# Kernel optimization log

Measured on AMD Instinct MI355X. Metric: run time of the kernel, lower is better.

## Reference

```python
import jax, jax.numpy as jnp
import numpy as np

N = 20000      # num_nodes
E = 256000     # num_edges (before self loops)
D_IN = 128
HID = 128      # hidden_dim (per-head out channels)
HEADS = 4
T = 2          # num_timesteps
NEG_SLOPE = 0.2
LN_EPS = 1e-5


def setup_inputs() -> dict:
    key = jax.random.key(0)
    ks = jax.random.split(key, 24)
    def rn(k, shape, s=0.05):
        return jax.random.normal(k, shape, jnp.float32) * s
    HH = HEADS * HID  # 512
    return {
        "x": jax.random.normal(ks[0], (N, D_IN), jnp.float32),
        "edge_index": jax.random.randint(ks[1], (2, E), 0, N),
        # input projection
        "Wp": rn(ks[2], (HID, D_IN)), "bp": jnp.zeros((HID,), jnp.float32),
        # GAT layer 0: in=HID, heads=HEADS, concat
        "W0": rn(ks[3], (HH, HID)), "as0": rn(ks[4], (HEADS, HID)), "ad0": rn(ks[5], (HEADS, HID)), "b0": jnp.zeros((HH,), jnp.float32),
        # GAT layer 1: in=HH, heads=HEADS, concat
        "W1": rn(ks[6], (HH, HH)), "as1": rn(ks[7], (HEADS, HID)), "ad1": rn(ks[8], (HEADS, HID)), "b1": jnp.zeros((HH,), jnp.float32),
        # GAT layer 2 (last): in=HH, heads=1, concat=False
        "W2": rn(ks[9], (HID, HH)), "as2": rn(ks[10], (1, HID)), "ad2": rn(ks[11], (1, HID)), "b2": jnp.zeros((HID,), jnp.float32),
        # layer norms (dims 512, 512, 128)
        "g0": jnp.ones((HH,), jnp.float32), "be0": jnp.zeros((HH,), jnp.float32),
        "g1": jnp.ones((HH,), jnp.float32), "be1": jnp.zeros((HH,), jnp.float32),
        "g2": jnp.ones((HID,), jnp.float32), "be2": jnp.zeros((HID,), jnp.float32),
        # temporal MultiheadAttention (embed=HID, 4 heads)
        "Wqkv": rn(ks[12], (3 * HID, HID)), "bqkv": jnp.zeros((3 * HID,), jnp.float32),
        "Wo": rn(ks[13], (HID, HID)), "bo": jnp.zeros((HID,), jnp.float32),
    }


def _layernorm(x, g, b):
    mu = x.mean(-1, keepdims=True)
    var = ((x - mu) ** 2).mean(-1, keepdims=True)
    return (x - mu) * jax.lax.rsqrt(var + LN_EPS) * g + b


def _gat_conv(h, src, dst, W, a_src, a_dst, bias, heads, concat):
    # h: [N, in]; W: [heads*HID, in]; a_src/a_dst: [heads, HID]
    xp = (h @ W.T).reshape(N, heads, HID)            # [N, heads, HID]
    al_s = (xp * a_src).sum(-1)                      # [N, heads]
    al_d = (xp * a_dst).sum(-1)                      # [N, heads]
    e = jax.nn.leaky_relu(al_s[src] + al_d[dst], NEG_SLOPE)  # [Etot, heads]
    m = jax.ops.segment_max(e, dst, num_segments=N)          # segment softmax over dst
    e = jnp.exp(e - m[dst])
    s = jax.ops.segment_sum(e, dst, num_segments=N)
    alpha = e / (s[dst] + 1e-16)                     # [Etot, heads]
    msg = xp[src] * alpha[:, :, None]                # [Etot, heads, HID]
    out = jax.ops.segment_sum(msg, dst, num_segments=N)      # [N, heads, HID]
    out = out.reshape(N, heads * HID) if concat else out.mean(1)
    return out + bias


def _forward(x, edge_index, Wp, bp, W0, as0, ad0, b0, W1, as1, ad1, b1,
             W2, as2, ad2, b2, g0, be0, g1, be1, g2, be2, Wqkv, bqkv, Wo, bo):
    loops = jnp.arange(N, dtype=edge_index.dtype)    # add_self_loops=True
    src = jnp.concatenate([edge_index[0], loops])
    dst = jnp.concatenate([edge_index[1], loops])

    h = x @ Wp.T + bp                                 # [N, HID]
    layers = [
        (W0, as0, ad0, b0, HEADS, True, g0, be0),
        (W1, as1, ad1, b1, HEADS, True, g1, be1),
        (W2, as2, ad2, b2, 1, False, g2, be2),
    ]
    states = []
    for t in range(T):
        h_t = h
        for i, (W, a_s, a_d, b, heads, concat, g, be) in enumerate(layers):
            h_res = h_t
            h_t = _gat_conv(h_t, src, dst, W, a_s, a_d, b, heads, concat)
            h_t = jax.nn.elu(h_t)
            h_t = _layernorm(h_t, g, be)
            # dropout is identity in eval mode
            if i > 0:
                if h_res.shape[-1] != h_t.shape[-1]:
                    # adaptive_avg_pool1d 512 -> 128: mean over groups of 4
                    r = h_res.shape[-1] // h_t.shape[-1]
                    h_res = h_res.reshape(N, h_t.shape[-1], r).mean(-1)
                h_t = h_t + h_res
        states.append(h_t)
        h = h_t

    ts = jnp.stack(states, axis=1)                    # [N, T, HID]
    # temporal self-attention (4 heads, head_dim = HID//4)
    nh, hd = 4, HID // 4
    qkv = ts @ Wqkv.T + bqkv                          # [N, T, 3*HID]
    q, k, v = jnp.split(qkv, 3, axis=-1)
    q = q.reshape(N, T, nh, hd).transpose(0, 2, 1, 3)
    k = k.reshape(N, T, nh, hd).transpose(0, 2, 1, 3)
    v = v.reshape(N, T, nh, hd).transpose(0, 2, 1, 3)
    attn = jax.nn.softmax(jnp.einsum("nhqd,nhkd->nhqk", q, k) / jnp.sqrt(jnp.float32(hd)), axis=-1)
    o = jnp.einsum("nhqk,nhkd->nhqd", attn, v).transpose(0, 2, 1, 3).reshape(N, T, HID)
    o = o @ Wo.T + bo
    return o.mean(axis=1)                             # [N, HID]


def reference(x, edge_index, Wp, bp, W0, as0, ad0, b0, W1, as1, ad1, b1,
              W2, as2, ad2, b2, g0, be0, g1, be1, g2, be2, Wqkv, bqkv, Wo, bo):
    return _forward(x, edge_index, Wp, bp, W0, as0, ad0, b0, W1, as1, ad1, b1,
                    W2, as2, ad2, b2, g0, be0, g1, be1, g2, be2, Wqkv, bqkv, Wo, bo)
```

## Files before the change

kernel.cpp:

```cpp
#include <hip/hip_runtime.h>
#include <math.h>

#define N_NODES 20000
#define N_EDGES 256000
#define ETOT (N_EDGES + N_NODES)
#define NPAD 20096
#define NPAD2 40064
#define NBLK_SCAN ((N_NODES + 255) / 256)

typedef __attribute__((ext_vector_type(8))) short bf16x8;
typedef __attribute__((ext_vector_type(4))) float f32x4;

__device__ __forceinline__ unsigned short f2bf(float f) {
    unsigned int u = __builtin_bit_cast(unsigned int, f);
    u = (u + 0x7fff + ((u >> 16) & 1)) >> 16;
    return (unsigned short)u;
}

__device__ __forceinline__ float bf2f(unsigned short u) {
    return __builtin_bit_cast(float, (unsigned int)u << 16);
}

__device__ __forceinline__ void gload_lds16(const void* g, void* l) {
    __builtin_amdgcn_global_load_lds(
        (const __attribute__((address_space(1))) void*)g,
        (__attribute__((address_space(3))) void*)l, 16, 0, 0);
}

__device__ __forceinline__ void fma8(float* acc, uint4 v, float w) {
    acc[0] = fmaf(w, __builtin_bit_cast(float, v.x << 16), acc[0]);
    acc[1] = fmaf(w, __builtin_bit_cast(float, v.x & 0xffff0000u), acc[1]);
    acc[2] = fmaf(w, __builtin_bit_cast(float, v.y << 16), acc[2]);
    acc[3] = fmaf(w, __builtin_bit_cast(float, v.y & 0xffff0000u), acc[3]);
    acc[4] = fmaf(w, __builtin_bit_cast(float, v.z << 16), acc[4]);
    acc[5] = fmaf(w, __builtin_bit_cast(float, v.z & 0xffff0000u), acc[5]);
    acc[6] = fmaf(w, __builtin_bit_cast(float, v.w << 16), acc[6]);
    acc[7] = fmaf(w, __builtin_bit_cast(float, v.w & 0xffff0000u), acc[7]);
}


__global__ void hist_kernel(const int* __restrict__ ei, int* __restrict__ cnt) {
    for (int e = blockIdx.x * blockDim.x + threadIdx.x; e < ETOT;
         e += gridDim.x * blockDim.x) {
        int d = (e < N_EDGES) ? ei[N_EDGES + e] : (e - N_EDGES);
        atomicAdd(&cnt[d], 1);
    }
}

__global__ __launch_bounds__(256) void scanA(const int* __restrict__ cnt,
                                             int* __restrict__ incl,
                                             int* __restrict__ bsum) {
    __shared__ int sh[256];
    int t = threadIdx.x;
    int i = blockIdx.x * 256 + t;
    int v = (i < N_NODES) ? cnt[i] : 0;
    sh[t] = v;
    __syncthreads();
#pragma unroll
    for (int off = 1; off < 256; off <<= 1) {
        int u = (t >= off) ? sh[t - off] : 0;
        __syncthreads();
        sh[t] += u;
        __syncthreads();
    }
    if (i < N_NODES) incl[i] = sh[t];
    if (t == 255) bsum[blockIdx.x] = sh[255];
}

__global__ __launch_bounds__(128) void scanB(int* __restrict__ bsum,
                                             int* __restrict__ row_start) {
    __shared__ int sh[128];
    int t = threadIdx.x;
    int v = (t < NBLK_SCAN) ? bsum[t] : 0;
    sh[t] = v;
    __syncthreads();
#pragma unroll
    for (int off = 1; off < 128; off <<= 1) {
        int u = (t >= off) ? sh[t - off] : 0;
        __syncthreads();
        sh[t] += u;
        __syncthreads();
    }
    if (t < NBLK_SCAN) bsum[t] = sh[t] - v;
    if (t == 0) row_start[0] = 0;
}

__global__ __launch_bounds__(256) void scanC(int* __restrict__ cursor,
                                             int* __restrict__ row_start,
                                             const int* __restrict__ bsum) {
    int i = blockIdx.x * 256 + threadIdx.x;
    if (i < N_NODES) {
        int incl = row_start[i + 1] + bsum[blockIdx.x];
        row_start[i + 1] = incl;
        cursor[i] = incl - cursor[i];
    }
}

__global__ void scatter_kernel(const int* __restrict__ ei, int* __restrict__ cursor,
                               int* __restrict__ sorted_id) {
    for (int e = blockIdx.x * blockDim.x + threadIdx.x; e < ETOT;
         e += gridDim.x * blockDim.x) {
        int d = (e < N_EDGES) ? ei[N_EDGES + e] : (e - N_EDGES);
        int pos = atomicAdd(&cursor[d], 1);
        sorted_id[pos] = e;
    }
}

__global__ __launch_bounds__(256) void segsort_kernel(
    const int* __restrict__ ei, const int* __restrict__ row_start,
    int* __restrict__ sorted_id, int* __restrict__ sorted_src) {
    int wv = threadIdx.x >> 6, lane = threadIdx.x & 63;
    int n = blockIdx.x * 4 + wv;
    if (n >= N_NODES) return;
    int base = row_start[n];
    int deg = row_start[n + 1] - base;
    if (deg <= 64) {
        int id = (lane < deg) ? sorted_id[base + lane] : 0x7fffffff;
        int rank = 0;
        for (int j = 0; j < deg; j++) {
            int idj = __shfl(id, j);
            rank += (idj < id);
        }
        if (lane < deg) {
            int src = (id < N_EDGES) ? ei[id] : (id - N_EDGES);
            sorted_src[base + rank] = src;
        }
    } else if (lane == 0) {
        for (int i = base + 1; i < base + deg; i++) {
            int v = sorted_id[i];
            int j = i - 1;
            while (j >= base && sorted_id[j] > v) {
                sorted_id[j + 1] = sorted_id[j];
                j--;
            }
            sorted_id[j + 1] = v;
        }
        for (int i = base; i < base + deg; i++) {
            int id = sorted_id[i];
            sorted_src[i] = (id < N_EDGES) ? ei[id] : (id - N_EDGES);
        }
    }
}

struct SetupArgs {
    const float* s[7];
    unsigned short* d[7];
    int cum[8];
    int* cursor;
    unsigned short* x16;
    unsigned short* h16n;
    unsigned short* h16wA;
    unsigned short* h16wB;
    unsigned short* xp16;
    unsigned short* st16;
    unsigned short* om16;
};

__global__ __launch_bounds__(256) void setup_all(SetupArgs a) {
    int i = blockIdx.x * 256 + threadIdx.x;
    const int PR = NPAD - N_NODES;
    if (i < N_NODES) a.cursor[i] = 0;
    if (i < PR * 128) {
        a.x16[(size_t)N_NODES * 128 + i] = 0;
        a.h16n[(size_t)N_NODES * 128 + i] = 0;
        a.om16[(size_t)N_NODES * 128 + i] = 0;
    }
    if (i < PR * 512) {
        a.h16wA[(size_t)N_NODES * 512 + i] = 0;
        a.h16wB[(size_t)N_NODES * 512 + i] = 0;
        a.xp16[(size_t)N_NODES * 512 + i] = 0;
    }
    if (i < (NPAD2 - 2 * N_NODES) * 128) a.st16[(size_t)(2 * N_NODES) * 128 + i] = 0;
    if (i < a.cum[7]) {
        int r = 0;
        while (i >= a.cum[r + 1]) r++;
        int off = i - a.cum[r];
        a.d[r][off] = f2bf(a.s[r][off]);
    }
}

__global__ __launch_bounds__(512) void make_ahat(
    const unsigned short* __restrict__ W016, const float* __restrict__ as0,
    const float* __restrict__ ad0, float* __restrict__ ahat_s,
    float* __restrict__ ahat_d) {
    int t = threadIdx.x;
    int h = t >> 7, k = t & 127;
    float ss = 0.f, sd = 0.f;
    for (int c = 0; c < 128; c++) {
        float w = bf2f(W016[(size_t)(h * 128 + c) * 128 + k]);
        ss = fmaf(as0[h * 128 + c], w, ss);
        sd = fmaf(ad0[h * 128 + c], w, sd);
    }
    ahat_s[t] = ss;
    ahat_d[t] = sd;
}

__global__ __launch_bounds__(256) void coef128(
    const unsigned short* __restrict__ h16n, const float* __restrict__ ahat_s,
    const float* __restrict__ ahat_d, float* __restrict__ als,
    float* __restrict__ ald) {
    int wv = threadIdx.x >> 6, lane = threadIdx.x & 63;
    int n = blockIdx.x * 4 + wv;
    if (n >= N_NODES) return;
    int k0 = 2 * lane;
    float h0 = bf2f(h16n[(size_t)n * 128 + k0]);
    float h1 = bf2f(h16n[(size_t)n * 128 + k0 + 1]);
    float accs[4], accd[4];
#pragma unroll
    for (int h = 0; h < 4; h++) {
        accs[h] = h0 * ahat_s[h * 128 + k0] + h1 * ahat_s[h * 128 + k0 + 1];
        accd[h] = h0 * ahat_d[h * 128 + k0] + h1 * ahat_d[h * 128 + k0 + 1];
    }
#pragma unroll
    for (int off = 1; off <= 32; off <<= 1) {
#pragma unroll
        for (int h = 0; h < 4; h++) {
            accs[h] += __shfl_xor(accs[h], off);
            accd[h] += __shfl_xor(accd[h], off);
        }
    }
    if (lane == 0) {
#pragma unroll
        for (int h = 0; h < 4; h++) {
            als[n * 4 + h] = accs[h];
            ald[n * 4 + h] = accd[h];
        }
    }
}

__global__ __launch_bounds__(256) void gemm_mfma(
    const unsigned short* __restrict__ A, const unsigned short* __restrict__ B,
    const float* __restrict__ bias, float* __restrict__ Cf,
    unsigned short* __restrict__ C16, int R, int K, int ldc,
    const float* __restrict__ a_s, const float* __restrict__ a_d,
    float* __restrict__ al_s, float* __restrict__ al_d, int H,
    int lda, int adiag) {
    __shared__ unsigned short Al[64 * 64];
    __shared__ unsigned short Bl[128 * 64];
    __shared__ float red_s[4][32], red_d[4][32];
    int tid = threadIdx.x;
    int lane = tid & 63, wv = tid >> 6;
    int wr = (wv >> 1) * 32, wc = (wv & 1) * 64;
    size_t br = (size_t)blockIdx.x * 64;
    size_t bc = (size_t)blockIdx.y * 128;
    int acol = adiag ? (int)blockIdx.y * K : 0;
    f32x4 acc[2][4] = {};
    for (int k0 = 0; k0 < K; k0 += 64) {
#pragma unroll
        for (int i = 0; i < 2; i++) {
            int idx = i * 256 + tid;
            int row = idx >> 3;
            int kb = (idx & 7) << 4;
            gload_lds16((const char*)(A + (br + row) * lda + acol + k0) + kb,
                        (char*)Al + idx * 16);
        }
#pragma unroll
        for (int i = 0; i < 4; i++) {
            int idx = i * 256 + tid;
            int row = idx >> 3;
            int kb = (idx & 7) << 4;
            gload_lds16((const char*)(B + (bc + row) * K + k0) + kb,
                        (char*)Bl + idx * 16);
        }
        __syncthreads();
#pragma unroll
        for (int kk = 0; kk < 2; kk++) {
            bf16x8 af[2], bfr[4];
#pragma unroll
            for (int m = 0; m < 2; m++)
                af[m] = *(const bf16x8*)&Al[(wr + m * 16 + (lane & 15)) * 64 +
                                            kk * 32 + (lane >> 4) * 8];
#pragma unroll
            for (int n = 0; n < 4; n++)
                bfr[n] = *(const bf16x8*)&Bl[(wc + n * 16 + (lane & 15)) * 64 +
                                             kk * 32 + (lane >> 4) * 8];
#pragma unroll
            for (int m = 0; m < 2; m++)
#pragma unroll
                for (int n = 0; n < 4; n++)
                    acc[m][n] = __builtin_amdgcn_mfma_f32_16x16x32_bf16(
                        af[m], bfr[n], acc[m][n], 0, 0, 0);
        }
        __syncthreads();
    }

    if (al_s) {
        float asr[4], adr[4];
#pragma unroll
        for (int n = 0; n < 4; n++) {
            int c = (int)bc + wc + n * 16 + (lane & 15);
            asr[n] = a_s[c];
            adr[n] = a_d[c];
        }
        float ps[2][4], pd[2][4];
#pragma unroll
        for (int m = 0; m < 2; m++)
#pragma unroll
            for (int j = 0; j < 4; j++) {
                float s = 0.f, d = 0.f;
#pragma unroll
                for (int n = 0; n < 4; n++) {
                    float v = acc[m][n][j];
                    s = fmaf(v, asr[n], s);
                    d = fmaf(v, adr[n], d);
                }
#pragma unroll
                for (int off = 8; off; off >>= 1) {
                    s += __shfl_xor(s, off);
                    d += __shfl_xor(d, off);
                }
                ps[m][j] = s;
                pd[m][j] = d;
            }
        if ((lane & 15) == 0) {
#pragma unroll
            for (int m = 0; m < 2; m++)
#pragma unroll
                for (int j = 0; j < 4; j++) {
                    int lr = m * 16 + (lane >> 4) * 4 + j;
                    red_s[wv][lr] = ps[m][j];
                    red_d[wv][lr] = pd[m][j];
                }
        }
        __syncthreads();
        if (tid < 64) {
            int half = tid >> 5, lr = tid & 31;
            float s = red_s[half * 2][lr] + red_s[half * 2 + 1][lr];
            float d = red_d[half * 2][lr] + red_d[half * 2 + 1][lr];
            size_t r = br + half * 32 + lr;
            if (r < (size_t)R) {
                al_s[r * H + blockIdx.y] = s;
                al_d[r * H + blockIdx.y] = d;
            }
        }
    }

#pragma unroll
    for (int m = 0; m < 2; m++) {
        int r0 = wr + m * 16 + (lane >> 4) * 4;
#pragma unroll
        for (int n = 0; n < 4; n++) {
            int c = (int)bc + wc + n * 16 + (lane & 15);
            float bv = bias ? bias[c] : 0.f;
#pragma unroll
            for (int j = 0; j < 4; j++) {
                size_t r = br + r0 + j;
                if (r < (size_t)R) {
                    float v = acc[m][n][j] + bv;
                    if (Cf) Cf[r * ldc + c] = v;
                    if (C16) C16[r * ldc + c] = f2bf(v);
                }
            }
        }
    }
}

template <int RES>
__global__ __launch_bounds__(256) void gat_agg512(
    const unsigned short* __restrict__ xp16, const float* __restrict__ al_s,
    const float* __restrict__ al_d, const int* __restrict__ row_start,
    const int* __restrict__ srcs, const float* __restrict__ bias,
    const float* __restrict__ gamma, const float* __restrict__ beta,
    const unsigned short* __restrict__ h_res16, unsigned short* __restrict__ out16) {
    const int C = 512;
    int tid = threadIdx.x;
    int lane = tid & 63, wv = tid >> 6;
    int n = blockIdx.x * 4 + wv;
    __shared__ int offw[4][64];
    __shared__ float logw[4][256];
    if (n >= N_NODES) return;
    int base = row_start[n];
    int deg = row_start[n + 1] - base;
    int head = lane >> 4;

    float acc[8] = {};
    float scale_end;

    if (deg <= 64) {
        int e_ = lane >> 2, h_ = lane & 3;
        float m = -3.4e38f;
        for (int e0 = 0; e0 < deg; e0 += 16) {
            int e = e0 + e_;
            float v = -3.4e38f;
            if (e < deg) {
                int src = srcs[base + e];
                if (h_ == 0) offw[wv][e] = src * (C * 2);
                float t = al_s[src * 4 + h_] + al_d[n * 4 + h_];
                v = t > 0.f ? t : 0.2f * t;
                logw[wv][e * 4 + h_] = v;
            }
            m = fmaxf(m, v);
        }
#pragma unroll
        for (int off = 4; off <= 32; off <<= 1) m = fmaxf(m, __shfl_xor(m, off));
        float s = 0.f;
        for (int e0 = 0; e0 < deg; e0 += 16) {
            int e = e0 + e_;
            if (e < deg) {
                float p = __expf(logw[wv][e * 4 + h_] - m);
                logw[wv][e * 4 + h_] = p;
                s += p;
            }
        }
#pragma unroll
        for (int off = 4; off <= 32; off <<= 1) s += __shfl_xor(s, off);
        float inv = 1.0f / (s + 1e-16f);
        scale_end = __shfl(inv, head);
        const char* xb = (const char*)xp16 + lane * 16;
#pragma unroll 4
        for (int j = 0; j < deg; j++) {
            float w = logw[wv][j * 4 + head];
            uint4 vv = *(const uint4*)(xb + offw[wv][j]);
            fma8(acc, vv, w);
        }
    } else {
        int e_ = lane >> 2, h_ = lane & 3;
        float m = -3.4e38f;
        for (int e0 = 0; e0 < deg; e0 += 16) {
            int e = e0 + e_;
            if (e < deg) {
                int src = srcs[base + e];
                float t = al_s[src * 4 + h_] + al_d[n * 4 + h_];
                t = t > 0.f ? t : 0.2f * t;
                m = fmaxf(m, t);
            }
        }
#pragma unroll
        for (int off = 4; off <= 32; off <<= 1) m = fmaxf(m, __shfl_xor(m, off));
        float s = 0.f;
        for (int e0 = 0; e0 < deg; e0 += 16) {
            int e = e0 + e_;
            if (e < deg) {
                int src = srcs[base + e];
                float t = al_s[src * 4 + h_] + al_d[n * 4 + h_];
                t = t > 0.f ? t : 0.2f * t;
                s += __expf(t - m);
            }
        }
#pragma unroll
        for (int off = 4; off <= 32; off <<= 1) s += __shfl_xor(s, off);
        float mg = __shfl(m, head);
        float sg = __shfl(s, head);
        float invg = 1.0f / (sg + 1e-16f);
        float aldh = al_d[n * 4 + head];
        const char* xb = (const char*)xp16 + lane * 16;
        for (int j = 0; j < deg; j++) {
            int src = srcs[base + j];
            float t = al_s[src * 4 + head] + aldh;
            t = t > 0.f ? t : 0.2f * t;
            float w = __expf(t - mg) * invg;
            uint4 vv = *(const uint4*)(xb + (size_t)src * (C * 2));
            fma8(acc, vv, w);
        }
        scale_end = 1.0f;
    }

    int ch0 = 8 * lane;
    float vals[8];
    {
        float4 b0 = *(const float4*)&bias[ch0];
        float4 b1 = *(const float4*)&bias[ch0 + 4];
        vals[0] = acc[0] * scale_end + b0.x;
        vals[1] = acc[1] * scale_end + b0.y;
        vals[2] = acc[2] * scale_end + b0.z;
        vals[3] = acc[3] * scale_end + b0.w;
        vals[4] = acc[4] * scale_end + b1.x;
        vals[5] = acc[5] * scale_end + b1.y;
        vals[6] = acc[6] * scale_end + b1.z;
        vals[7] = acc[7] * scale_end + b1.w;
    }
    float s2 = 0.f, q = 0.f;
#pragma unroll
    for (int k = 0; k < 8; k++) {
        vals[k] = vals[k] > 0.f ? vals[k] : (__expf(vals[k]) - 1.0f);
        s2 += vals[k];
        q += vals[k] * vals[k];
    }
#pragma unroll
    for (int off = 1; off <= 32; off <<= 1) {
        s2 += __shfl_xor(s2, off);
        q += __shfl_xor(q, off);
    }
    float mu = s2 / C;
    float var = q / C - mu * mu;
    float rstd = 1.0f / sqrtf(var + 1e-5f);
    {
        float4 g0 = *(const float4*)&gamma[ch0];
        float4 g1 = *(const float4*)&gamma[ch0 + 4];
        float4 be0v = *(const float4*)&beta[ch0];
        float4 be1v = *(const float4*)&beta[ch0 + 4];
        float gg[8] = {g0.x, g0.y, g0.z, g0.w, g1.x, g1.y, g1.z, g1.w};
        float bb[8] = {be0v.x, be0v.y, be0v.z, be0v.w,
                       be1v.x, be1v.y, be1v.z, be1v.w};
#pragma unroll
        for (int k = 0; k < 8; k++) vals[k] = (vals[k] - mu) * rstd * gg[k] + bb[k];
    }
    if (RES == 1) {
        ushort4 r0 = *(const ushort4*)&h_res16[(size_t)n * C + ch0];
        ushort4 r1 = *(const ushort4*)&h_res16[(size_t)n * C + ch0 + 4];
        vals[0] += bf2f(r0.x); vals[1] += bf2f(r0.y);
        vals[2] += bf2f(r0.z); vals[3] += bf2f(r0.w);
        vals[4] += bf2f(r1.x); vals[5] += bf2f(r1.y);
        vals[6] += bf2f(r1.z); vals[7] += bf2f(r1.w);
    }
    uint4 pk;
    pk.x = (unsigned)f2bf(vals[0]) | ((unsigned)f2bf(vals[1]) << 16);
    pk.y = (unsigned)f2bf(vals[2]) | ((unsigned)f2bf(vals[3]) << 16);
    pk.z = (unsigned)f2bf(vals[4]) | ((unsigned)f2bf(vals[5]) << 16);
    pk.w = (unsigned)f2bf(vals[6]) | ((unsigned)f2bf(vals[7]) << 16);
    *(uint4*)&out16[(size_t)n * C + ch0] = pk;
}

__global__ __launch_bounds__(256) void gat_gather128(
    const unsigned short* __restrict__ h16n, const float* __restrict__ al_s,
    const float* __restrict__ al_d, const int* __restrict__ row_start,
    const int* __restrict__ srcs, unsigned short* __restrict__ s16) {
    int tid = threadIdx.x;
    int lane = tid & 63, wv = tid >> 6;
    int n = blockIdx.x * 4 + wv;
    __shared__ int offw[4][64];
    __shared__ float logw[4][256];
    if (n >= N_NODES) return;
    int base = row_start[n];
    int deg = row_start[n + 1] - base;
    int head = lane >> 4;
    int li = lane & 15;

    float acc[8] = {};
    float scale_end;

    if (deg <= 64) {
        int e_ = lane >> 2, h_ = lane & 3;
        float m = -3.4e38f;
        for (int e0 = 0; e0 < deg; e0 += 16) {
            int e = e0 + e_;
            float v = -3.4e38f;
            if (e < deg) {
                int src = srcs[base + e];
                if (h_ == 0) offw[wv][e] = src * 256;
                float t = al_s[src * 4 + h_] + al_d[n * 4 + h_];
                v = t > 0.f ? t : 0.2f * t;
                logw[wv][e * 4 + h_] = v;
            }
            m = fmaxf(m, v);
        }
#pragma unroll
        for (int off = 4; off <= 32; off <<= 1) m = fmaxf(m, __shfl_xor(m, off));
        float s = 0.f;
        for (int e0 = 0; e0 < deg; e0 += 16) {
            int e = e0 + e_;
            if (e < deg) {
                float p = __expf(logw[wv][e * 4 + h_] - m);
                logw[wv][e * 4 + h_] = p;
                s += p;
            }
        }
#pragma unroll
        for (int off = 4; off <= 32; off <<= 1) s += __shfl_xor(s, off);
        float inv = 1.0f / (s + 1e-16f);
        scale_end = __shfl(inv, head);
        const char* xb = (const char*)h16n + li * 16;
#pragma unroll 4
        for (int j = 0; j < deg; j++) {
            float w = logw[wv][j * 4 + head];
            uint4 vv = *(const uint4*)(xb + offw[wv][j]);
            fma8(acc, vv, w);
        }
    } else {
        int e_ = lane >> 2, h_ = lane & 3;
        float m = -3.4e38f;
        for (int e0 = 0; e0 < deg; e0 += 16) {
            int e = e0 + e_;
            if (e < deg) {
                int src = srcs[base + e];
                float t = al_s[src * 4 + h_] + al_d[n * 4 + h_];
                t = t > 0.f ? t : 0.2f * t;
                m = fmaxf(m, t);
            }
        }
#pragma unroll
        for (int off = 4; off <= 32; off <<= 1) m = fmaxf(m, __shfl_xor(m, off));
        float s = 0.f;
        for (int e0 = 0; e0 < deg; e0 += 16) {
            int e = e0 + e_;
            if (e < deg) {
                int src = srcs[base + e];
                float t = al_s[src * 4 + h_] + al_d[n * 4 + h_];
                t = t > 0.f ? t : 0.2f * t;
                s += __expf(t - m);
            }
        }
#pragma unroll
        for (int off = 4; off <= 32; off <<= 1) s += __shfl_xor(s, off);
        float mg = __shfl(m, head);
        float sg = __shfl(s, head);
        float invg = 1.0f / (sg + 1e-16f);
        float aldh = al_d[n * 4 + head];
        const char* xb = (const char*)h16n + li * 16;
        for (int j = 0; j < deg; j++) {
            int src = srcs[base + j];
            float t = al_s[src * 4 + head] + aldh;
            t = t > 0.f ? t : 0.2f * t;
            float w = __expf(t - mg) * invg;
            uint4 vv = *(const uint4*)(xb + (size_t)src * 256);
            fma8(acc, vv, w);
        }
        scale_end = 1.0f;
    }

    uint4 pk;
    pk.x = (unsigned)f2bf(acc[0] * scale_end) | ((unsigned)f2bf(acc[1] * scale_end) << 16);
    pk.y = (unsigned)f2bf(acc[2] * scale_end) | ((unsigned)f2bf(acc[3] * scale_end) << 16);
    pk.z = (unsigned)f2bf(acc[4] * scale_end) | ((unsigned)f2bf(acc[5] * scale_end) << 16);
    pk.w = (unsigned)f2bf(acc[6] * scale_end) | ((unsigned)f2bf(acc[7] * scale_end) << 16);
    *(uint4*)&s16[(size_t)n * 512 + 8 * lane] = pk;
}

__global__ __launch_bounds__(256) void ln512(
    const unsigned short* __restrict__ proj16, const float* __restrict__ bias,
    const float* __restrict__ gamma, const float* __restrict__ beta,
    unsigned short* __restrict__ out16) {
    const int C = 512;
    int lane = threadIdx.x & 63, wv = threadIdx.x >> 6;
    int n = blockIdx.x * 4 + wv;
    if (n >= N_NODES) return;
    int ch0 = 8 * lane;
    uint4 pv = *(const uint4*)&proj16[(size_t)n * C + ch0];
    float4 b0 = *(const float4*)&bias[ch0];
    float4 b1 = *(const float4*)&bias[ch0 + 4];
    float vals[8];
    vals[0] = __builtin_bit_cast(float, pv.x << 16) + b0.x;
    vals[1] = __builtin_bit_cast(float, pv.x & 0xffff0000u) + b0.y;
    vals[2] = __builtin_bit_cast(float, pv.y << 16) + b0.z;
    vals[3] = __builtin_bit_cast(float, pv.y & 0xffff0000u) + b0.w;
    vals[4] = __builtin_bit_cast(float, pv.z << 16) + b1.x;
    vals[5] = __builtin_bit_cast(float, pv.z & 0xffff0000u) + b1.y;
    vals[6] = __builtin_bit_cast(float, pv.w << 16) + b1.z;
    vals[7] = __builtin_bit_cast(float, pv.w & 0xffff0000u) + b1.w;
    float s2 = 0.f, q = 0.f;
#pragma unroll
    for (int k = 0; k < 8; k++) {
        vals[k] = vals[k] > 0.f ? vals[k] : (__expf(vals[k]) - 1.0f);
        s2 += vals[k];
        q += vals[k] * vals[k];
    }
#pragma unroll
    for (int off = 1; off <= 32; off <<= 1) {
        s2 += __shfl_xor(s2, off);
        q += __shfl_xor(q, off);
    }
    float mu = s2 / C;
    float var = q / C - mu * mu;
    float rstd = 1.0f / sqrtf(var + 1e-5f);
    float4 g0 = *(const float4*)&gamma[ch0];
    float4 g1 = *(const float4*)&gamma[ch0 + 4];
    float4 be0v = *(const float4*)&beta[ch0];
    float4 be1v = *(const float4*)&beta[ch0 + 4];
    float gg[8] = {g0.x, g0.y, g0.z, g0.w, g1.x, g1.y, g1.z, g1.w};
    float bb[8] = {be0v.x, be0v.y, be0v.z, be0v.w, be1v.x, be1v.y, be1v.z, be1v.w};
#pragma unroll
    for (int k = 0; k < 8; k++) vals[k] = (vals[k] - mu) * rstd * gg[k] + bb[k];
    uint4 pk;
    pk.x = (unsigned)f2bf(vals[0]) | ((unsigned)f2bf(vals[1]) << 16);
    pk.y = (unsigned)f2bf(vals[2]) | ((unsigned)f2bf(vals[3]) << 16);
    pk.z = (unsigned)f2bf(vals[4]) | ((unsigned)f2bf(vals[5]) << 16);
    pk.w = (unsigned)f2bf(vals[6]) | ((unsigned)f2bf(vals[7]) << 16);
    *(uint4*)&out16[(size_t)n * C + ch0] = pk;
}

__global__ __launch_bounds__(64) void gat_agg128(
    const unsigned short* __restrict__ xp16, const float* __restrict__ al_s,
    const float* __restrict__ al_d, const int* __restrict__ row_start,
    const int* __restrict__ srcs, const float* __restrict__ bias,
    const float* __restrict__ gamma, const float* __restrict__ beta,
    const unsigned short* __restrict__ h_res16, unsigned short* __restrict__ out16,
    unsigned short* __restrict__ out2_16, int out2_stride) {
    const int C = 128;
    int n = blockIdx.x;
    int lane = threadIdx.x & 63;
    __shared__ int off_sh[64];
    __shared__ float w_sh[64];
    __shared__ float m_sh, s_sh;
    int base = row_start[n];
    int deg = row_start[n + 1] - base;

    float acc[8] = {};

    if (deg <= 64) {
        float v = -3.4e38f;
        if (lane < deg) {
            int src = srcs[base + lane];
            off_sh[lane] = src * (C * 2);
            float t = al_s[src] + al_d[n];
            v = t > 0.f ? t : 0.2f * t;
        }
        float m = v;
#pragma unroll
        for (int off = 32; off; off >>= 1) m = fmaxf(m, __shfl_xor(m, off));
        float p = (lane < deg) ? __expf(v - m) : 0.f;
        float s = p;
#pragma unroll
        for (int off = 32; off; off >>= 1) s += __shfl_xor(s, off);
        s += 1e-16f;
        if (lane < deg) w_sh[lane] = p / s;
        __syncthreads();
        int li = lane & 15, rg = lane >> 4;
        const char* xb = (const char*)xp16 + li * 16;
        for (int j = rg; j < deg; j += 4) {
            uint4 vv = *(const uint4*)(xb + off_sh[j]);
            fma8(acc, vv, w_sh[j]);
        }
    } else {
        float ald = al_d[n];
        float m = -3.4e38f;
        for (int e = lane; e < deg; e += 64) {
            float v = al_s[srcs[base + e]] + ald;
            v = v > 0.f ? v : 0.2f * v;
            m = fmaxf(m, v);
        }
#pragma unroll
        for (int off = 32; off; off >>= 1) m = fmaxf(m, __shfl_xor(m, off));
        float s = 0.f;
        for (int e = lane; e < deg; e += 64) {
            float v = al_s[srcs[base + e]] + ald;
            v = v > 0.f ? v : 0.2f * v;
            s += __expf(v - m);
        }
#pragma unroll
        for (int off = 32; off; off >>= 1) s += __shfl_xor(s, off);
        if (lane == 0) { m_sh = m; s_sh = s + 1e-16f; }
        __syncthreads();
        float mh = m_sh, ssh = s_sh;
        int li = lane & 15, rg = lane >> 4;
        const char* xb = (const char*)xp16 + li * 16;
        for (int j = rg; j < deg; j += 4) {
            int src = srcs[base + j];
            float t = al_s[src] + ald;
            t = t > 0.f ? t : 0.2f * t;
            float w = __expf(t - mh) / ssh;
            uint4 vv = *(const uint4*)(xb + (size_t)src * (C * 2));
            fma8(acc, vv, w);
        }
    }

#pragma unroll
    for (int k = 0; k < 8; k++) {
        acc[k] += __shfl_xor(acc[k], 16);
        acc[k] += __shfl_xor(acc[k], 32);
    }
    int li = lane & 15;
    int ch0 = 8 * li;
    float vals[8];
    float4 b0 = *(const float4*)&bias[ch0];
    float4 b1 = *(const float4*)&bias[ch0 + 4];
    vals[0] = acc[0] + b0.x; vals[1] = acc[1] + b0.y;
    vals[2] = acc[2] + b0.z; vals[3] = acc[3] + b0.w;
    vals[4] = acc[4] + b1.x; vals[5] = acc[5] + b1.y;
    vals[6] = acc[6] + b1.z; vals[7] = acc[7] + b1.w;
    float s = 0.f, q = 0.f;
#pragma unroll
    for (int k = 0; k < 8; k++) {
        vals[k] = vals[k] > 0.f ? vals[k] : (__expf(vals[k]) - 1.0f);
        s += vals[k];
        q += vals[k] * vals[k];
    }
#pragma unroll
    for (int off = 8; off; off >>= 1) {
        s += __shfl_xor(s, off);
        q += __shfl_xor(q, off);
    }
    float mu = s / C;
    float var = q / C - mu * mu;
    float rstd = 1.0f / sqrtf(var + 1e-5f);
    float4 g0 = *(const float4*)&gamma[ch0];
    float4 g1 = *(const float4*)&gamma[ch0 + 4];
    float4 be0v = *(const float4*)&beta[ch0];
    float4 be1v = *(const float4*)&beta[ch0 + 4];
    float gg[8] = {g0.x, g0.y, g0.z, g0.w, g1.x, g1.y, g1.z, g1.w};
    float bb[8] = {be0v.x, be0v.y, be0v.z, be0v.w, be1v.x, be1v.y, be1v.z, be1v.w};
#pragma unroll
    for (int k = 0; k < 8; k++) vals[k] = (vals[k] - mu) * rstd * gg[k] + bb[k];
    {
        const unsigned short* r = &h_res16[(size_t)n * 512 + 4 * ch0];
#pragma unroll
        for (int k = 0; k < 8; k++) {
            ushort4 rv = *(const ushort4*)&r[4 * k];
            vals[k] += 0.25f * (bf2f(rv.x) + bf2f(rv.y) + bf2f(rv.z) + bf2f(rv.w));
        }
    }
    if (lane < 16) {
        uint4 pk;
        pk.x = (unsigned)f2bf(vals[0]) | ((unsigned)f2bf(vals[1]) << 16);
        pk.y = (unsigned)f2bf(vals[2]) | ((unsigned)f2bf(vals[3]) << 16);
        pk.z = (unsigned)f2bf(vals[4]) | ((unsigned)f2bf(vals[5]) << 16);
        pk.w = (unsigned)f2bf(vals[6]) | ((unsigned)f2bf(vals[7]) << 16);
        if (out16) *(uint4*)&out16[(size_t)n * C + ch0] = pk;
        if (out2_16) *(uint4*)&out2_16[(size_t)n * out2_stride + ch0] = pk;
    }
}

__global__ __launch_bounds__(128) void temporal_attn(
    const unsigned short* __restrict__ qkv16, unsigned short* __restrict__ om16) {
    __shared__ float sh[768];
    int n = blockIdx.x;
    int c = threadIdx.x;
    for (int i = c; i < 768; i += 128) {
        int t = i / 384;
        sh[i] = bf2f(qkv16[(size_t)(n * 2 + t) * 384 + (i - t * 384)]);
    }
    __syncthreads();
    int head = c >> 5;
    int hb = head * 32;
    const float scale = 0.17677669529663687f;
    float o[2];
#pragma unroll
    for (int qt = 0; qt < 2; qt++) {
        float s0 = 0.f, s1 = 0.f;
#pragma unroll
        for (int d = 0; d < 32; d++) {
            float qv = sh[qt * 384 + hb + d];
            s0 = fmaf(qv, sh[0 * 384 + 128 + hb + d], s0);
            s1 = fmaf(qv, sh[1 * 384 + 128 + hb + d], s1);
        }
        s0 *= scale; s1 *= scale;
        float m = fmaxf(s0, s1);
        float p0 = __expf(s0 - m), p1 = __expf(s1 - m);
        float inv = 1.0f / (p0 + p1);
        o[qt] = p0 * inv * sh[0 * 384 + 256 + c] + p1 * inv * sh[1 * 384 + 256 + c];
    }
    om16[(size_t)n * 128 + c] = f2bf(0.5f * (o[0] + o[1]));
}


extern "C" void kernel_launch(void* const* d_in, const int* in_sizes, int n_in,
                              void* d_out, int out_size, void* d_ws, size_t ws_size,
                              hipStream_t stream) {
    const float* x   = (const float*)d_in[0];
    const int*   ei  = (const int*)d_in[1];
    const float* Wp  = (const float*)d_in[2];
    const float* bp  = (const float*)d_in[3];
    const float* W0  = (const float*)d_in[4];
    const float* as0 = (const float*)d_in[5];
    const float* ad0 = (const float*)d_in[6];
    const float* b0  = (const float*)d_in[7];
    const float* W1  = (const float*)d_in[8];
    const float* as1 = (const float*)d_in[9];
    const float* ad1 = (const float*)d_in[10];
    const float* b1  = (const float*)d_in[11];
    const float* W2  = (const float*)d_in[12];
    const float* as2 = (const float*)d_in[13];
    const float* ad2 = (const float*)d_in[14];
    const float* b2  = (const float*)d_in[15];
    const float* g0  = (const float*)d_in[16];
    const float* be0 = (const float*)d_in[17];
    const float* g1  = (const float*)d_in[18];
    const float* be1 = (const float*)d_in[19];
    const float* g2  = (const float*)d_in[20];
    const float* be2 = (const float*)d_in[21];
    const float* Wqkv = (const float*)d_in[22];
    const float* bqkv = (const float*)d_in[23];
    const float* Wo  = (const float*)d_in[24];
    const float* bo  = (const float*)d_in[25];
    float* out = (float*)d_out;

    const int N = N_NODES;
    float* f = (float*)d_ws;
    float* als = f;
    float* ald = als + (size_t)N * 4;
    float* ahat_s = ald + (size_t)N * 4;
    float* ahat_d = ahat_s + 512;
    int* row_start  = (int*)(ahat_d + 512);
    int* cursor     = row_start + (N + 1);
    int* sorted_id  = cursor + N;
    int* sorted_src = sorted_id + ETOT;
    int* bsum       = sorted_src + ETOT;
    uintptr_t pa = (uintptr_t)(bsum + NBLK_SCAN + 1);
    pa = (pa + 63) & ~(uintptr_t)63;
    unsigned short* x16   = (unsigned short*)pa;
    unsigned short* h16n  = x16 + (size_t)NPAD * 128;
    unsigned short* h16wA = h16n + (size_t)NPAD * 128;
    unsigned short* h16wB = h16wA + (size_t)NPAD * 512;
    unsigned short* xp16  = h16wB + (size_t)NPAD * 512;
    unsigned short* st16  = xp16 + (size_t)NPAD * 512;
    unsigned short* qkv16 = st16 + (size_t)NPAD2 * 128;
    unsigned short* om16  = qkv16 + (size_t)NPAD2 * 384;
    unsigned short* w16   = om16 + (size_t)NPAD * 128;
    unsigned short* Wp16   = w16;
    unsigned short* W016   = Wp16 + 128 * 128;
    unsigned short* W116   = W016 + 512 * 128;
    unsigned short* W216   = W116 + 512 * 512;
    unsigned short* Wqkv16 = W216 + 128 * 512;
    unsigned short* Wo16   = Wqkv16 + 384 * 128;

    {
        SetupArgs a;
        const float* srcs7[7] = {Wp, W0, W1, W2, Wqkv, Wo, x};
        unsigned short* dsts7[7] = {Wp16, W016, W116, W216, Wqkv16, Wo16, x16};
        int sizes7[7] = {128 * 128, 512 * 128, 512 * 512, 128 * 512,
                         384 * 128, 128 * 128, N_NODES * 128};
        int c = 0;
        a.cum[0] = 0;
        for (int i = 0; i < 7; i++) {
            a.s[i] = srcs7[i];
            a.d[i] = dsts7[i];
            c += sizes7[i];
            a.cum[i + 1] = c;
        }
        a.cursor = cursor;
        a.x16 = x16; a.h16n = h16n; a.h16wA = h16wA; a.h16wB = h16wB;
        a.xp16 = xp16; a.st16 = st16; a.om16 = om16;
        setup_all<<<(c + 255) / 256, 256, 0, stream>>>(a);
    }
    make_ahat<<<1, 512, 0, stream>>>(W016, as0, ad0, ahat_s, ahat_d);

    hist_kernel<<<1024, 256, 0, stream>>>(ei, cursor);
    scanA<<<NBLK_SCAN, 256, 0, stream>>>(cursor, row_start + 1, bsum);
    scanB<<<1, 128, 0, stream>>>(bsum, row_start);
    scanC<<<NBLK_SCAN, 256, 0, stream>>>(cursor, row_start, bsum);
    scatter_kernel<<<1024, 256, 0, stream>>>(ei, cursor, sorted_id);
    segsort_kernel<<<(N + 3) / 4, 256, 0, stream>>>(ei, row_start, sorted_id,
                                                    sorted_src);

    const int GX = NPAD / 64;
    const int GX2 = NPAD2 / 64;
    const int GA = (N + 3) / 4;
    {
        dim3 g(GX, 1);
        gemm_mfma<<<g, 256, 0, stream>>>(x16, Wp16, bp, nullptr, h16n, N, 128, 128,
                                         nullptr, nullptr, nullptr, nullptr, 0,
                                         128, 0);
    }

    for (int t = 0; t < 2; t++) {
        {
            coef128<<<GA, 256, 0, stream>>>(h16n, ahat_s, ahat_d, als, ald);
            gat_gather128<<<GA, 256, 0, stream>>>(h16n, als, ald, row_start,
                                                  sorted_src, xp16);
            dim3 g(GX, 4);
            gemm_mfma<<<g, 256, 0, stream>>>(xp16, W016, nullptr, nullptr, h16wB,
                                             N, 128, 512, nullptr, nullptr,
                                             nullptr, nullptr, 0, 512, 1);
            ln512<<<GA, 256, 0, stream>>>(h16wB, b0, g0, be0, h16wA);
        }
        {
            dim3 g(GX, 4);
            gemm_mfma<<<g, 256, 0, stream>>>(h16wA, W116, nullptr, nullptr, xp16,
                                             N, 512, 512, as1, ad1, als, ald, 4,
                                             512, 0);
            gat_agg512<1><<<GA, 256, 0, stream>>>(
                xp16, als, ald, row_start, sorted_src, b1, g1, be1, h16wA, h16wB);
        }
        {
            dim3 g(GX, 1);
            gemm_mfma<<<g, 256, 0, stream>>>(h16wB, W216, nullptr, nullptr, xp16,
                                             N, 512, 128, as2, ad2, als, ald, 1,
                                             512, 0);
            gat_agg128<<<N, 64, 0, stream>>>(
                xp16, als, ald, row_start, sorted_src, b2, g2, be2, h16wB,
                (t == 0) ? h16n : nullptr, st16 + (size_t)t * 128, 256);
        }
    }

    {
        dim3 g(GX2, 3);
        gemm_mfma<<<g, 256, 0, stream>>>(st16, Wqkv16, bqkv, nullptr, qkv16,
                                         2 * N, 128, 384, nullptr, nullptr,
                                         nullptr, nullptr, 0, 128, 0);
    }
    temporal_attn<<<N, 128, 0, stream>>>(qkv16, om16);
    {
        dim3 g(GX, 1);
        gemm_mfma<<<g, 256, 0, stream>>>(om16, Wo16, bo, out, nullptr,
                                         N, 128, 128, nullptr, nullptr,
                                         nullptr, nullptr, 0, 128, 0);
    }
}
```

Baseline: 474.8 us.

## Split edges across lane groups in gat_gather128 and reduce heads by shuffles

In the 128-wide GAT gather, each 16-lane group used to walk every edge for its own head, so all four groups loaded the same source row. Now each group takes every fourth edge and accumulates all four heads from a single 16-byte load. It reads the per-edge weights as a float4, and the high-degree path computes all four head weights at once. A cross-group shuffle reduction then combines the partial sums and each lane selects its head. This cuts redundant gathers and sequential loop trips, at the cost of four times the accumulator registers, more FMAs per load, and 64 extra shuffles per node.

```diff
diff --git a/kernel.cpp b/kernel.cpp
--- a/kernel.cpp
+++ b/kernel.cpp
@@ -525,9 +525,10 @@
     int deg = row_start[n + 1] - base;
     int head = lane >> 4;
     int li = lane & 15;
-
-    float acc[8] = {};
-    float scale_end;
+    int rg = lane >> 4;
+
+    float acc0[8] = {}, acc1[8] = {}, acc2[8] = {}, acc3[8] = {};
+    float scale_end = 1.0f;
 
     if (deg <= 64) {
         int e_ = lane >> 2, h_ = lane & 3;
@@ -560,11 +561,14 @@
         float inv = 1.0f / (s + 1e-16f);
         scale_end = __shfl(inv, head);
         const char* xb = (const char*)h16n + li * 16;
-#pragma unroll 4
-        for (int j = 0; j < deg; j++) {
-            float w = logw[wv][j * 4 + head];
+#pragma unroll 2
+        for (int j = rg; j < deg; j += 4) {
+            float4 w4 = *(const float4*)&logw[wv][j * 4];
             uint4 vv = *(const uint4*)(xb + offw[wv][j]);
-            fma8(acc, vv, w);
+            fma8(acc0, vv, w4.x);
+            fma8(acc1, vv, w4.y);
+            fma8(acc2, vv, w4.z);
+            fma8(acc3, vv, w4.w);
         }
     } else {
         int e_ = lane >> 2, h_ = lane & 3;
@@ -592,27 +596,51 @@
         }
 #pragma unroll
         for (int off = 4; off <= 32; off <<= 1) s += __shfl_xor(s, off);
-        float mg = __shfl(m, head);
-        float sg = __shfl(s, head);
-        float invg = 1.0f / (sg + 1e-16f);
-        float aldh = al_d[n * 4 + head];
+        float mg0 = __shfl(m, 0), mg1 = __shfl(m, 1);
+        float mg2 = __shfl(m, 2), mg3 = __shfl(m, 3);
+        float iv0 = 1.0f / (__shfl(s, 0) + 1e-16f);
+        float iv1 = 1.0f / (__shfl(s, 1) + 1e-16f);
+        float iv2 = 1.0f / (__shfl(s, 2) + 1e-16f);
+        float iv3 = 1.0f / (__shfl(s, 3) + 1e-16f);
+        float4 adv = *(const float4*)&al_d[n * 4];
         const char* xb = (const char*)h16n + li * 16;
-        for (int j = 0; j < deg; j++) {
+        for (int j = rg; j < deg; j += 4) {
             int src = srcs[base + j];
-            float t = al_s[src * 4 + head] + aldh;
-            t = t > 0.f ? t : 0.2f * t;
-            float w = __expf(t - mg) * invg;
+            float4 asv = *(const float4*)&al_s[src * 4];
+            float t0 = asv.x + adv.x; t0 = t0 > 0.f ? t0 : 0.2f * t0;
+            float t1 = asv.y + adv.y; t1 = t1 > 0.f ? t1 : 0.2f * t1;
+            float t2 = asv.z + adv.z; t2 = t2 > 0.f ? t2 : 0.2f * t2;
+            float t3 = asv.w + adv.w; t3 = t3 > 0.f ? t3 : 0.2f * t3;
             uint4 vv = *(const uint4*)(xb + (size_t)src * 256);
-            fma8(acc, vv, w);
+            fma8(acc0, vv, __expf(t0 - mg0) * iv0);
+            fma8(acc1, vv, __expf(t1 - mg1) * iv1);
+            fma8(acc2, vv, __expf(t2 - mg2) * iv2);
+            fma8(acc3, vv, __expf(t3 - mg3) * iv3);
         }
         scale_end = 1.0f;
     }
 
+#pragma unroll
+    for (int k = 0; k < 8; k++) {
+        acc0[k] += __shfl_xor(acc0[k], 16); acc0[k] += __shfl_xor(acc0[k], 32);
+        acc1[k] += __shfl_xor(acc1[k], 16); acc1[k] += __shfl_xor(acc1[k], 32);
+        acc2[k] += __shfl_xor(acc2[k], 16); acc2[k] += __shfl_xor(acc2[k], 32);
+        acc3[k] += __shfl_xor(acc3[k], 16); acc3[k] += __shfl_xor(acc3[k], 32);
+    }
+    float out[8];
+#pragma unroll
+    for (int k = 0; k < 8; k++) {
+        float v = head == 0 ? acc0[k]
+                : head == 1 ? acc1[k]
+                : head == 2 ? acc2[k]
+                            : acc3[k];
+        out[k] = v * scale_end;
+    }
     uint4 pk;
-    pk.x = (unsigned)f2bf(acc[0] * scale_end) | ((unsigned)f2bf(acc[1] * scale_end) << 16);
-    pk.y = (unsigned)f2bf(acc[2] * scale_end) | ((unsigned)f2bf(acc[3] * scale_end) << 16);
-    pk.z = (unsigned)f2bf(acc[4] * scale_end) | ((unsigned)f2bf(acc[5] * scale_end) << 16);
-    pk.w = (unsigned)f2bf(acc[6] * scale_end) | ((unsigned)f2bf(acc[7] * scale_end) << 16);
+    pk.x = (unsigned)f2bf(out[0]) | ((unsigned)f2bf(out[1]) << 16);
+    pk.y = (unsigned)f2bf(out[2]) | ((unsigned)f2bf(out[3]) << 16);
+    pk.z = (unsigned)f2bf(out[4]) | ((unsigned)f2bf(out[5]) << 16);
+    pk.w = (unsigned)f2bf(out[6]) | ((unsigned)f2bf(out[7]) << 16);
     *(uint4*)&s16[(size_t)n * 512 + 8 * lane] = pk;
 }
 
```

After: 491.1 us. 3.4% more time.
